# Optimization experiments

Hardware: AMD Instinct MI355X
Metric: run time of the kernel (lower is better)

The kernel has to match this reference:

```python
import jax, jax.numpy as jnp
import numpy as np

EPS = 1e-6
NEG_SLOPE = 0.01  # torch LeakyReLU default

def ln(x, g, b):
    m = jnp.mean(x, axis=-1, keepdims=True)
    v = jnp.mean((x - m) ** 2, axis=-1, keepdims=True)
    return (x - m) / jnp.sqrt(v + EPS) * g + b

def leaky(x):
    return jnp.where(x >= 0, x, NEG_SLOPE * x)

def setup_inputs() -> dict:
    B, L, F, H, NH, LBL = 8, 1024, 1024, 256, 8, 4766
    key = jax.random.key(0)
    ks = jax.random.split(key, 16)
    def lin(k, i, o, s=0.03):
        kw, kb = jax.random.split(k)
        return jax.random.normal(kw, (i, o), jnp.float32) * s, jnp.zeros((o,), jnp.float32)
    w_in, b_in = lin(ks[0], F, H)
    w_h, b_h = lin(ks[1], H, H)
    a_w1, a_b1 = lin(ks[2], H, 64)
    a_w2, a_b2 = lin(ks[3], 64, NH)
    o_w1, o_b1 = lin(ks[4], NH * H, NH * H)
    o_w2, o_b2 = lin(ks[5], NH * H, LBL)
    CM = (jax.random.uniform(ks[6], (LBL, LBL)) < 0.002).astype(jnp.float32)
    CM = jnp.maximum(CM, jnp.eye(LBL, dtype=jnp.float32))
    return {
        'h_V': jax.random.normal(ks[7], (B, L, F), jnp.float32),
        'mask': jnp.ones((B, L), jnp.int32),
        'ln0_g': jnp.ones((F,), jnp.float32), 'ln0_b': jnp.zeros((F,), jnp.float32),
        'w_in': w_in, 'b_in': b_in,
        'ln1_g': jnp.ones((H,), jnp.float32), 'ln1_b': jnp.zeros((H,), jnp.float32),
        'w_h': w_h, 'b_h': b_h,
        'ln2_g': jnp.ones((H,), jnp.float32), 'ln2_b': jnp.zeros((H,), jnp.float32),
        'a_w1': a_w1, 'a_b1': a_b1,
        'a_lng': jnp.ones((64,), jnp.float32), 'a_lnb': jnp.zeros((64,), jnp.float32),
        'a_w2': a_w2, 'a_b2': a_b2,
        'o_w1': o_w1, 'o_b1': o_b1,
        'o_lng': jnp.ones((NH * H,), jnp.float32), 'o_lnb': jnp.zeros((NH * H,), jnp.float32),
        'o_w2': o_w2, 'o_b2': o_b2,
        'CM': CM,
    }

def reference(h_V, mask, ln0_g, ln0_b, w_in, b_in, ln1_g, ln1_b, w_h, b_h,
              ln2_g, ln2_b, a_w1, a_b1, a_lng, a_lnb, a_w2, a_b2,
              o_w1, o_b1, o_lng, o_lnb, o_w2, o_b2, CM):
    B = h_V.shape[0]
    # input + hidden blocks (eval mode: dropout is identity)
    x = ln(h_V, ln0_g, ln0_b)
    x = leaky(x @ w_in + b_in)
    x = ln(x, ln1_g, ln1_b)
    x = leaky(x @ w_h + b_h)
    x = ln(x, ln2_g, ln2_b)                      # [B,L,H]
    # multi-head attention pooling over sequence
    a = leaky(x @ a_w1 + a_b1)
    a = ln(a, a_lng, a_lnb)
    a = a @ a_w2 + a_b2                          # [B,L,NH]
    a = jnp.where(mask[:, :, None] == 0, jnp.float32(-1e9), a)
    a = jax.nn.softmax(a, axis=1)
    h = jnp.einsum('blh,bld->bhd', a, x).reshape(B, -1)  # [B,NH*H]
    # output block
    h = leaky(h @ o_w1 + o_b1)
    h = ln(h, o_lng, o_lnb)
    p = jax.nn.sigmoid(h @ o_w2 + o_b2)          # [B,LBL]
    # GO-hierarchy max-product propagation (eval path)
    out = jnp.max(p[:, None, :] * CM[None, :, :], axis=-1)  # [B,LBL]
    return out.astype(jnp.float32)
```

## Files before the change

kernel.cpp:

```cpp
#include <hip/hip_runtime.h>
#include <hip/hip_bf16.h>
#include <cstdint>

#define B_   8
#define L_   1024
#define F_   1024
#define H_   256
#define NH_  8
#define LBL_ 4766
#define M_   (B_*L_)
#define OD_  (NH_*H_)
#define NCM  (LBL_*LBL_)
#define MP_EPB 16384
#define MP_NB  ((NCM + MP_EPB - 1) / MP_EPB)

typedef unsigned short u16;
typedef unsigned int   u32;
typedef __attribute__((ext_vector_type(8))) short short8;
typedef __attribute__((ext_vector_type(4))) float float4v;

#define BF16_ONES_PAIR 0x3f803f80u

__device__ __forceinline__ float bf2f(u32 u) { return __uint_as_float(u << 16); }
__device__ __forceinline__ u16 f2bf(float f) {
    u32 u = __float_as_uint(f);
    u32 r = 0x7fffu + ((u >> 16) & 1u);
    return (u16)((u + r) >> 16);
}

struct f8 { float v[8]; };

__device__ __forceinline__ float ldS(const void* p, size_t i, bool bf) {
    return bf ? bf2f(((const u16*)p)[i]) : ((const float*)p)[i];
}
__device__ __forceinline__ float4 ld4(const void* p, size_t i, bool bf) {
    if (bf) {
        uint2 u = *(const uint2*)((const u16*)p + i);
        return make_float4(bf2f(u.x & 0xffff), bf2f(u.x >> 16),
                           bf2f(u.y & 0xffff), bf2f(u.y >> 16));
    }
    return *(const float4*)((const float*)p + i);
}
__device__ __forceinline__ f8 ld8(const void* p, size_t i, bool bf) {
    f8 r;
    if (bf) {
        uint4 u = *(const uint4*)((const u16*)p + i);
        r.v[0]=bf2f(u.x&0xffff); r.v[1]=bf2f(u.x>>16);
        r.v[2]=bf2f(u.y&0xffff); r.v[3]=bf2f(u.y>>16);
        r.v[4]=bf2f(u.z&0xffff); r.v[5]=bf2f(u.z>>16);
        r.v[6]=bf2f(u.w&0xffff); r.v[7]=bf2f(u.w>>16);
    } else {
        const float* q = (const float*)p + i;
        float4 a = *(const float4*)q, b = *(const float4*)(q+4);
        r.v[0]=a.x; r.v[1]=a.y; r.v[2]=a.z; r.v[3]=a.w;
        r.v[4]=b.x; r.v[5]=b.y; r.v[6]=b.z; r.v[7]=b.w;
    }
    return r;
}

__device__ __forceinline__ float wave_sum(float v) {
    #pragma unroll
    for (int m = 1; m < 64; m <<= 1) v += __shfl_xor(v, m, 64);
    return v;
}
__device__ __forceinline__ float wave_max(float v) {
    #pragma unroll
    for (int m = 1; m < 64; m <<= 1) v = fmaxf(v, __shfl_xor(v, m, 64));
    return v;
}
__device__ __forceinline__ float blk_sum(float v, float* sh) {
    v = wave_sum(v);
    int w = threadIdx.x >> 6, nw = blockDim.x >> 6;
    if ((threadIdx.x & 63) == 0) sh[w] = v;
    __syncthreads();
    float s = sh[0];
    for (int i = 1; i < nw; ++i) s += sh[i];
    __syncthreads();
    return s;
}
__device__ __forceinline__ float blk_max(float v, float* sh) {
    v = wave_max(v);
    int w = threadIdx.x >> 6, nw = blockDim.x >> 6;
    if ((threadIdx.x & 63) == 0) sh[w] = v;
    __syncthreads();
    float s = sh[0];
    for (int i = 1; i < nw; ++i) s = fmaxf(s, sh[i]);
    __syncthreads();
    return s;
}

__global__ __launch_bounds__(256) void prep_k(const void* __restrict__ hv,
        const void* __restrict__ g0, const void* __restrict__ b0, u16* __restrict__ x0,
        const void* __restrict__ w_in, u16* __restrict__ wt1,
        const void* __restrict__ w_h,  u16* __restrict__ wt2,
        const void* __restrict__ aw1,  u16* __restrict__ wt3,
        float* __restrict__ zA, float* __restrict__ zB,
        const u32* __restrict__ probe) {
    __shared__ u16 tile[64][65];
    __shared__ float sh[4];
    bool bf = (probe[0] == BF16_ONES_PAIR);
    int blk = blockIdx.x, t = threadIdx.x;
    if (blk < M_) {
        float4 v = ld4(hv, (size_t)blk * F_ + t * 4, bf);
        float s = v.x + v.y + v.z + v.w;
        float q = v.x*v.x + v.y*v.y + v.z*v.z + v.w*v.w;
        s = blk_sum(s, sh);
        q = blk_sum(q, sh);
        float mean = s * (1.f / F_);
        float rstd = rsqrtf(q * (1.f / F_) - mean * mean + 1e-6f);
        float4 gg = ld4(g0, t * 4, bf);
        float4 bb = ld4(b0, t * 4, bf);
        u32 o0 = f2bf((v.x - mean) * rstd * gg.x + bb.x)
               | ((u32)f2bf((v.y - mean) * rstd * gg.y + bb.y) << 16);
        u32 o1 = f2bf((v.z - mean) * rstd * gg.z + bb.z)
               | ((u32)f2bf((v.w - mean) * rstd * gg.w + bb.w) << 16);
        *(uint2*)(x0 + (size_t)blk * F_ + t * 4) = make_uint2(o0, o1);
        return;
    }
    blk -= M_;
    const void* W = nullptr; u16* WT = nullptr; int K = 0, N = 0, kt = 0, nt = 0;
    if (blk < 64)      { W = w_in; WT = wt1; K = F_; N = H_; kt = blk & 15; nt = blk >> 4; }
    else if (blk < 80) { int j = blk - 64; W = w_h; WT = wt2; K = H_; N = H_; kt = j & 3; nt = j >> 2; }
    else if (blk < 84) { int j = blk - 80; W = aw1; WT = wt3; K = H_; N = 64; kt = j; nt = 0; }
    else {
        int j = blk - 84;
        if (j < 16) {
            float4* p = (float4*)zA;
            for (int i = j * 256 + t; i < 8192; i += 4096) p[i] = make_float4(0,0,0,0);
        } else {
            j -= 16;
            float4* p = (float4*)zB;
            for (int i = j * 256 + t; i < 13628; i += 4096) p[i] = make_float4(0,0,0,0);
        }
        return;
    }
    int kt0 = kt * 64, nt0 = nt * 64;
    int r = t >> 2, cq = (t & 3) * 16;
    #pragma unroll
    for (int j = 0; j < 4; ++j) {
        float4 v = ld4(W, (size_t)(kt0 + r) * N + nt0 + cq + j * 4, bf);
        tile[r][cq + j*4 + 0] = f2bf(v.x);
        tile[r][cq + j*4 + 1] = f2bf(v.y);
        tile[r][cq + j*4 + 2] = f2bf(v.z);
        tile[r][cq + j*4 + 3] = f2bf(v.w);
    }
    __syncthreads();
    #pragma unroll
    for (int j = 0; j < 4; ++j) {
        int k = cq + j * 4;
        u32 a0 = tile[k+0][r], a1 = tile[k+1][r], a2 = tile[k+2][r], a3 = tile[k+3][r];
        uint2 o; o.x = a0 | (a1 << 16); o.y = a2 | (a3 << 16);
        *(uint2*)(WT + (size_t)(nt0 + r) * K + kt0 + k) = o;
    }
}

__global__ __launch_bounds__(256) void gemm_mfma(const u16* __restrict__ Ap, int amode,
        const float2* __restrict__ statin, const void* __restrict__ g,
        const void* __restrict__ bta, const u16* __restrict__ WT,
        const void* __restrict__ bias, u16* __restrict__ C,
        float* __restrict__ statout, int M, int N, int K,
        const u32* __restrict__ probe) {
    __shared__ short8 As[64][5];
    __shared__ short8 Bs[64][5];
    bool pbf = (probe[0] == BF16_ONES_PAIR);
    int t = threadIdx.x;
    int m0 = blockIdx.x * 64, n0 = blockIdx.y * 64;
    int r = t >> 2, kq = t & 3;
    int l = t & 63, w = t >> 6;
    int q = l >> 4, ml = l & 15;
    float4v acc[4];
    #pragma unroll
    for (int nt = 0; nt < 4; ++nt)
        #pragma unroll
        for (int i = 0; i < 4; ++i) acc[nt][i] = 0.f;
    float stm = 0.f, str = 1.f;
    if (amode == 1) {
        float2 st = statin[m0 + r];
        float mm = st.x * (1.f / K);
        stm = mm;
        str = rsqrtf(st.y * (1.f / K) - mm * mm + 1e-6f);
    }
    for (int k0 = 0; k0 < K; k0 += 32) {
        int kk = k0 + kq * 8;
        short8 pa;
        if (amode == 1) {
            f8 a  = ld8(Ap, (size_t)(m0 + r) * K + kk, true);
            f8 gg = ld8(g, kk, pbf);
            f8 bb = ld8(bta, kk, pbf);
            #pragma unroll
            for (int j = 0; j < 8; ++j)
                pa[j] = (short)f2bf((a.v[j] - stm) * str * gg.v[j] + bb.v[j]);
        } else {
            pa = *(const short8*)(Ap + (size_t)(m0 + r) * K + kk);
        }
        short8 pb = *(const short8*)(WT + (size_t)(n0 + r) * K + kk);
        __syncthreads();
        As[r][kq] = pa;
        Bs[r][kq] = pb;
        __syncthreads();
        short8 af = As[w * 16 + ml][q];
        #pragma unroll
        for (int nt = 0; nt < 4; ++nt)
            acc[nt] = __builtin_amdgcn_mfma_f32_16x16x32_bf16(af, Bs[nt*16 + ml][q],
                                                              acc[nt], 0, 0, 0);
    }
    float ov[4][4];
    #pragma unroll
    for (int nt = 0; nt < 4; ++nt) {
        int nn = n0 + nt * 16 + ml;
        float bv = ldS(bias, nn, pbf);
        #pragma unroll
        for (int reg = 0; reg < 4; ++reg) {
            float v = acc[nt][reg] + bv;
            v = v >= 0.f ? v : 0.01f * v;
            ov[nt][reg] = v;
            C[(size_t)(m0 + w * 16 + q * 4 + reg) * N + nn] = f2bf(v);
        }
    }
    if (statout) {
        #pragma unroll
        for (int reg = 0; reg < 4; ++reg) {
            float sv = ov[0][reg] + ov[1][reg] + ov[2][reg] + ov[3][reg];
            float qv = ov[0][reg]*ov[0][reg] + ov[1][reg]*ov[1][reg]
                     + ov[2][reg]*ov[2][reg] + ov[3][reg]*ov[3][reg];
            #pragma unroll
            for (int mk = 1; mk < 16; mk <<= 1) {
                sv += __shfl_xor(sv, mk, 64);
                qv += __shfl_xor(qv, mk, 64);
            }
            if (ml == 0) {
                int row = m0 + w * 16 + q * 4 + reg;
                atomicAdd(&statout[2 * row],     sv);
                atomicAdd(&statout[2 * row + 1], qv);
            }
        }
    }
}

__global__ __launch_bounds__(256) void gemm3_attn_k(const u16* __restrict__ Ap,
        const float2* __restrict__ statin, const void* __restrict__ g,
        const void* __restrict__ bta, const u16* __restrict__ WT,
        const void* __restrict__ bias,
        const void* __restrict__ alng, const void* __restrict__ alnb,
        const void* __restrict__ aw2, const void* __restrict__ ab2,
        const int* __restrict__ mask, float* __restrict__ lg,
        const u32* __restrict__ probe) {
    __shared__ short8 As[64][5];
    __shared__ short8 Bs[64][5];
    __shared__ float at[64][65];
    __shared__ float w2s[512];
    __shared__ float b2s[8];
    __shared__ float gs[64], bs[64];
    bool pbf = (probe[0] == BF16_ONES_PAIR);
    const int K = 256;
    int t = threadIdx.x;
    int m0 = blockIdx.x * 64;
    int r = t >> 2, kq = t & 3;
    int l = t & 63, w = t >> 6;
    int q = l >> 4, ml = l & 15;
    float4v acc[4];
    #pragma unroll
    for (int nt = 0; nt < 4; ++nt)
        #pragma unroll
        for (int i = 0; i < 4; ++i) acc[nt][i] = 0.f;
    float2 st = statin[m0 + r];
    float stm = st.x * (1.f / K);
    float str = rsqrtf(st.y * (1.f / K) - stm * stm + 1e-6f);
    for (int k0 = 0; k0 < K; k0 += 32) {
        int kk = k0 + kq * 8;
        f8 a  = ld8(Ap, (size_t)(m0 + r) * K + kk, true);
        f8 gg = ld8(g, kk, pbf);
        f8 bb = ld8(bta, kk, pbf);
        short8 pa;
        #pragma unroll
        for (int j = 0; j < 8; ++j)
            pa[j] = (short)f2bf((a.v[j] - stm) * str * gg.v[j] + bb.v[j]);
        short8 pb = *(const short8*)(WT + (size_t)r * K + kk);
        __syncthreads();
        As[r][kq] = pa;
        Bs[r][kq] = pb;
        __syncthreads();
        short8 af = As[w * 16 + ml][q];
        #pragma unroll
        for (int nt = 0; nt < 4; ++nt)
            acc[nt] = __builtin_amdgcn_mfma_f32_16x16x32_bf16(af, Bs[nt*16 + ml][q],
                                                              acc[nt], 0, 0, 0);
    }
    for (int i = t; i < 512; i += 256) w2s[i] = ldS(aw2, i, pbf);
    if (t < 8) b2s[t] = ldS(ab2, t, pbf);
    if (t < 64) { gs[t] = ldS(alng, t, pbf); bs[t] = ldS(alnb, t, pbf); }
    #pragma unroll
    for (int nt = 0; nt < 4; ++nt) {
        int nn = nt * 16 + ml;
        float bv = ldS(bias, nn, pbf);
        #pragma unroll
        for (int reg = 0; reg < 4; ++reg) {
            float v = acc[nt][reg] + bv;
            v = v >= 0.f ? v : 0.01f * v;
            at[w * 16 + q * 4 + reg][nn] = v;
        }
    }
    __syncthreads();
    int row = t >> 2, s4 = t & 3;
    float av[16];
    float sum = 0.f, sq = 0.f;
    #pragma unroll
    for (int j = 0; j < 16; ++j) {
        float v = at[row][s4 * 16 + j];
        av[j] = v; sum += v; sq += v * v;
    }
    sum += __shfl_xor(sum, 1, 64); sum += __shfl_xor(sum, 2, 64);
    sq  += __shfl_xor(sq, 1, 64);  sq  += __shfl_xor(sq, 2, 64);
    float mr = sum * (1.f / 64);
    float rr = rsqrtf(sq * (1.f / 64) - mr * mr + 1e-6f);
    float val[16];
    #pragma unroll
    for (int j = 0; j < 16; ++j)
        val[j] = (av[j] - mr) * rr * gs[s4 * 16 + j] + bs[s4 * 16 + j];
    float hv[8];
    #pragma unroll
    for (int h = 0; h < 8; ++h) {
        float p = 0.f;
        #pragma unroll
        for (int j = 0; j < 16; ++j) p += val[j] * w2s[(s4 * 16 + j) * 8 + h];
        p += __shfl_xor(p, 1, 64);
        p += __shfl_xor(p, 2, 64);
        hv[h] = p + b2s[h];
    }
    if (s4 == 0) {
        int gr = m0 + row;
        bool mz = (mask[gr] == 0);
        int bb_ = gr >> 10, ll = gr & 1023;
        #pragma unroll
        for (int h = 0; h < 8; ++h) {
            float v = mz ? -1e9f : hv[h];
            lg[((size_t)bb_ * NH_ + h) * L_ + ll] = v;
        }
    }
}

__global__ __launch_bounds__(1024) void attnpool_k(const float* __restrict__ lg,
        const float2* __restrict__ st2, const u16* __restrict__ x2,
        const void* __restrict__ g, const void* __restrict__ b,
        float* __restrict__ hp, const u32* __restrict__ probe) {
    __shared__ float aw_s[1024];
    __shared__ float part[16][256];
    __shared__ float sh[16];
    bool pbf = (probe[0] == BF16_ONES_PAIR);
    int bh = blockIdx.x, t = threadIdx.x;
    int bb = bh >> 3;
    float v = lg[(size_t)bh * L_ + t];
    float mx = blk_max(v, sh);
    float e = expf(v - mx);
    float s = blk_sum(e, sh);
    float inv = 1.f / s;
    float2 st = st2[(bb << 10) + t];
    float m = st.x * (1.f / 256);
    float r = rsqrtf(st.y * (1.f / 256) - m * m + 1e-6f);
    float aw = e * inv * r;
    aw_s[t] = aw;
    float c1 = blk_sum(aw * m, sh);
    int chunk = t >> 6, d0 = (t & 63) * 4;
    const u16* xb = x2 + ((size_t)(bb << 10) + chunk * 64) * 256;
    const float* awc = aw_s + chunk * 64;
    float a0 = 0.f, a1 = 0.f, a2 = 0.f, a3 = 0.f;
    #pragma unroll 8
    for (int i = 0; i < 64; ++i) {
        uint2 u = *(const uint2*)(xb + (size_t)i * 256 + d0);
        float wv = awc[i];
        a0 += wv * bf2f(u.x & 0xffff);
        a1 += wv * bf2f(u.x >> 16);
        a2 += wv * bf2f(u.y & 0xffff);
        a3 += wv * bf2f(u.y >> 16);
    }
    *(float4*)&part[chunk][d0] = make_float4(a0, a1, a2, a3);
    __syncthreads();
    if (t < 256) {
        float S = 0.f;
        #pragma unroll
        for (int c = 0; c < 16; ++c) S += part[c][t];
        hp[(size_t)bh * 256 + t] = (S - c1) * ldS(g, t, pbf) + ldS(b, t, pbf);
    }
}

__global__ __launch_bounds__(256) void gemv2_k(const float* __restrict__ hv,
        const void* __restrict__ W, float* __restrict__ acc, int K, int N,
        const u32* __restrict__ probe) {
    __shared__ float hs[8 * 64];
    bool bf = (probe[0] == BF16_ONES_PAIR);
    int t = threadIdx.x;
    int kb = blockIdx.y * 64;
    for (int i = t; i < 512; i += 256) {
        int r = i >> 6, k = i & 63;
        hs[i] = hv[(size_t)r * K + kb + k];
    }
    __syncthreads();
    int c0 = (blockIdx.x * 256 + t) * 2;
    if (c0 >= N) return;
    float a[8][2] = {};
    #pragma unroll 4
    for (int k = 0; k < 64; ++k) {
        float w0, w1;
        if (bf) {
            u32 u = *(const u32*)((const u16*)W + (size_t)(kb + k) * N + c0);
            w0 = bf2f(u & 0xffff); w1 = bf2f(u >> 16);
        } else {
            float2 fw = *(const float2*)((const float*)W + (size_t)(kb + k) * N + c0);
            w0 = fw.x; w1 = fw.y;
        }
        #pragma unroll
        for (int r = 0; r < 8; ++r) {
            float h = hs[(r << 6) + k];
            a[r][0] += h * w0; a[r][1] += h * w1;
        }
    }
    bool ok1 = (c0 + 1 < N);
    #pragma unroll
    for (int r = 0; r < 8; ++r) {
        atomicAdd(&acc[(size_t)r * N + c0], a[r][0]);
        if (ok1) atomicAdd(&acc[(size_t)r * N + c0 + 1], a[r][1]);
    }
}

__global__ __launch_bounds__(256) void out_ln_k(float* __restrict__ h,
        const void* __restrict__ bias, const void* __restrict__ g,
        const void* __restrict__ b, const u32* __restrict__ probe) {
    __shared__ float sh[4];
    bool bf = (probe[0] == BF16_ONES_PAIR);
    int row = blockIdx.x, t = threadIdx.x;
    float v[8];
    float s = 0.f, q = 0.f;
    #pragma unroll
    for (int i = 0; i < 8; ++i) {
        int c = t + i * 256;
        float x = h[(size_t)row * OD_ + c] + ldS(bias, c, bf);
        x = x >= 0.f ? x : 0.01f * x;
        v[i] = x; s += x; q += x * x;
    }
    s = blk_sum(s, sh) * (1.f / OD_);
    q = blk_sum(q, sh) * (1.f / OD_);
    float rstd = rsqrtf(q - s * s + 1e-6f);
    #pragma unroll
    for (int i = 0; i < 8; ++i) {
        int c = t + i * 256;
        h[(size_t)row * OD_ + c] = (v[i] - s) * rstd * ldS(g, c, bf) + ldS(b, c, bf);
    }
}

__global__ __launch_bounds__(256) void sigmoid_t_k(const float* __restrict__ acc,
        const void* __restrict__ bias, float* __restrict__ pt,
        float* __restrict__ out, const u32* __restrict__ probe) {
    bool bf = (probe[0] == BF16_ONES_PAIR);
    int c = blockIdx.x * 256 + threadIdx.x;
    if (c >= LBL_) return;
    float bv = ldS(bias, c, bf);
    float o[8];
    #pragma unroll
    for (int r = 0; r < 8; ++r) {
        float v = acc[(size_t)r * LBL_ + c] + bv;
        o[r] = 1.f / (1.f + expf(-v));
        out[(size_t)r * LBL_ + c] = 0.f;
    }
    float4* dst = (float4*)(pt + (size_t)c * 8);
    dst[0] = make_float4(o[0], o[1], o[2], o[3]);
    dst[1] = make_float4(o[4], o[5], o[6], o[7]);
}

__device__ __forceinline__ void mp_hit(u32 idx, float cmv,
        const float* __restrict__ pt, int* smax, u32 rowBase) {
    u32 i = idx / LBL_;
    u32 j = idx - i * LBL_;
    const float4* pj = (const float4*)(pt + (size_t)j * 8);
    float4 pa = pj[0], pb = pj[1];
    int base = (int)(i - rowBase) * 8;
    atomicMax(&smax[base + 0], __float_as_int(pa.x * cmv));
    atomicMax(&smax[base + 1], __float_as_int(pa.y * cmv));
    atomicMax(&smax[base + 2], __float_as_int(pa.z * cmv));
    atomicMax(&smax[base + 3], __float_as_int(pa.w * cmv));
    atomicMax(&smax[base + 4], __float_as_int(pb.x * cmv));
    atomicMax(&smax[base + 5], __float_as_int(pb.y * cmv));
    atomicMax(&smax[base + 6], __float_as_int(pb.z * cmv));
    atomicMax(&smax[base + 7], __float_as_int(pb.w * cmv));
}

__global__ __launch_bounds__(256) void maxprod3_k(const float* __restrict__ pt,
        const void* __restrict__ CM, float* __restrict__ out,
        const u32* __restrict__ probe) {
    __shared__ int smax[6 * 8];
    bool bf = (probe[0] == BF16_ONES_PAIR);
    int t = threadIdx.x;
    size_t blockStart = (size_t)blockIdx.x * MP_EPB;
    u32 rowBase = (u32)(blockStart / LBL_);
    for (int i = t; i < 48; i += 256) smax[i] = 0;
    __syncthreads();
    if (bf) {
        const u16* cm = (const u16*)CM;
        uint4 ch[8];
        size_t i0[8];
        #pragma unroll
        for (int u = 0; u < 8; ++u) {
            size_t idx0 = blockStart + ((size_t)u * 256 + t) * 8;
            i0[u] = idx0;
            ch[u] = (idx0 + 8 <= NCM) ? *(const uint4*)(cm + idx0)
                                      : make_uint4(0, 0, 0, 0);
        }
        #pragma unroll
        for (int u = 0; u < 8; ++u) {
            size_t idx0 = i0[u];
            if (idx0 + 8 <= NCM) {
                uint4 c4 = ch[u];
                if ((c4.x | c4.y | c4.z | c4.w) == 0) continue;
                u32 hw[4] = {c4.x, c4.y, c4.z, c4.w};
                #pragma unroll
                for (int d = 0; d < 4; ++d) {
                    u32 lo = hw[d] & 0xffff, hi = hw[d] >> 16;
                    if (lo) mp_hit((u32)idx0 + d*2,     bf2f(lo), pt, smax, rowBase);
                    if (hi) mp_hit((u32)idx0 + d*2 + 1, bf2f(hi), pt, smax, rowBase);
                }
            } else if (idx0 < NCM) {
                for (u32 e = 0; e < (u32)(NCM - idx0); ++e) {
                    u16 h = cm[idx0 + e];
                    if (h) mp_hit((u32)idx0 + e, bf2f(h), pt, smax, rowBase);
                }
            }
        }
    } else {
        const float* cm = (const float*)CM;
        #pragma unroll
        for (int u = 0; u < 16; ++u) {
            size_t idx0 = blockStart + ((size_t)u * 256 + t) * 4;
            if (idx0 >= NCM) continue;
            float v[4];
            if (idx0 + 4 <= NCM) {
                float4 f = *(const float4*)(cm + idx0);
                v[0] = f.x; v[1] = f.y; v[2] = f.z; v[3] = f.w;
            } else {
                v[0] = v[1] = v[2] = v[3] = 0.f;
                for (u32 e = 0; e < (u32)(NCM - idx0); ++e) v[e] = cm[idx0 + e];
            }
            if (v[0] == 0.f && v[1] == 0.f && v[2] == 0.f && v[3] == 0.f) continue;
            #pragma unroll
            for (int e = 0; e < 4; ++e)
                if (v[e] != 0.f) mp_hit((u32)idx0 + e, v[e], pt, smax, rowBase);
        }
    }
    __syncthreads();
    size_t lastIdx = blockStart + MP_EPB - 1;
    if (lastIdx >= NCM) lastIdx = NCM - 1;
    int nrows = (int)((u32)(lastIdx / LBL_) - rowBase) + 1;
    for (int s = t; s < nrows * 8; s += 256) {
        int v = smax[s];
        if (v != 0) {
            int rr = s >> 3, b = s & 7;
            atomicMax((int*)(out + (size_t)b * LBL_ + rowBase + rr), v);
        }
    }
}

extern "C" void kernel_launch(void* const* d_in, const int* in_sizes, int n_in,
                              void* d_out, int out_size, void* d_ws, size_t ws_size,
                              hipStream_t stream) {
    const void* hv   = d_in[0];
    const int* mask  = (const int*)d_in[1];
    const void* ln0g = d_in[2];
    const void* ln0b = d_in[3];
    const void* w_in = d_in[4];
    const void* b_in = d_in[5];
    const void* ln1g = d_in[6];
    const void* ln1b = d_in[7];
    const void* w_h  = d_in[8];
    const void* b_h  = d_in[9];
    const void* ln2g = d_in[10];
    const void* ln2b = d_in[11];
    const void* aw1  = d_in[12];
    const void* ab1  = d_in[13];
    const void* alng = d_in[14];
    const void* alnb = d_in[15];
    const void* aw2  = d_in[16];
    const void* ab2  = d_in[17];
    const void* ow1  = d_in[18];
    const void* ob1  = d_in[19];
    const void* olng = d_in[20];
    const void* olnb = d_in[21];
    const void* ow2  = d_in[22];
    const void* ob2  = d_in[23];
    const void* CM   = d_in[24];
    const u32* probe = (const u32*)ln0g;
    float* out = (float*)d_out;

    float* f = (float*)d_ws;
    float2* st1 = (float2*)f;
    float2* st2 = st1 + 8192;
    float* lg = f + 32768;
    float* c1 = lg + 65536;
    float* Sp = c1 + 64;
    float* hp = Sp + 131072;
    float* ha = hp + 16384;
    float* l2 = ha + 16384;
    float* pt = l2 + 38128;
    u16* x0  = (u16*)(pt + 38128);
    u16* x1  = x0 + 8388608;
    u16* x2  = x1 + 2097152;
    u16* abr = x2 + 2097152;
    u16* wt1 = abr + 524288;
    u16* wt2 = wt1 + 262144;
    u16* wt3 = wt2 + 65536;

    prep_k<<<M_ + 84 + 32, 256, 0, stream>>>(hv, ln0g, ln0b, x0,
                                             w_in, wt1, w_h, wt2, aw1, wt3,
                                             f, ha, probe);
    gemm_mfma<<<dim3(M_/64, 4), 256, 0, stream>>>(x0, 2, nullptr, nullptr, nullptr,
                                                  wt1, b_in, x1, (float*)st1,
                                                  M_, H_, F_, probe);
    gemm_mfma<<<dim3(M_/64, 4), 256, 0, stream>>>(x1, 1, st1, ln1g, ln1b,
                                                  wt2, b_h, x2, (float*)st2,
                                                  M_, H_, H_, probe);
    gemm3_attn_k<<<M_/64, 256, 0, stream>>>(x2, st2, ln2g, ln2b, wt3, ab1,
                                            alng, alnb, aw2, ab2, mask, lg, probe);
    attnpool_k<<<B_*NH_, 1024, 0, stream>>>(lg, st2, x2, ln2g, ln2b, hp, probe);
    gemv2_k<<<dim3(OD_/512, 32), 256, 0, stream>>>(hp, ow1, ha, OD_, OD_, probe);
    out_ln_k<<<B_, 256, 0, stream>>>(ha, ob1, olng, olnb, probe);
    gemv2_k<<<dim3((LBL_+511)/512, 32), 256, 0, stream>>>(ha, ow2, l2, OD_, LBL_, probe);
    sigmoid_t_k<<<(LBL_+255)/256, 256, 0, stream>>>(l2, ob2, pt, out, probe);
    maxprod3_k<<<MP_NB, 256, 0, stream>>>(pt, CM, out, probe);
}
```

Baseline: 353.7 us.

## Double-buffer GEMM LDS tiles, wave-per-row input LayerNorm, 4-wide output GEMV

```diff
diff --git a/kernel.cpp b/kernel.cpp
--- a/kernel.cpp
+++ b/kernel.cpp
@@ -97,27 +97,40 @@
         float* __restrict__ zA, float* __restrict__ zB,
         const u32* __restrict__ probe) {
     __shared__ u16 tile[64][65];
-    __shared__ float sh[4];
     bool bf = (probe[0] == BF16_ONES_PAIR);
     int blk = blockIdx.x, t = threadIdx.x;
-    if (blk < M_) {
-        float4 v = ld4(hv, (size_t)blk * F_ + t * 4, bf);
-        float s = v.x + v.y + v.z + v.w;
-        float q = v.x*v.x + v.y*v.y + v.z*v.z + v.w*v.w;
-        s = blk_sum(s, sh);
-        q = blk_sum(q, sh);
+    if (blk < M_/4) {
+        int row = (blk << 2) + (t >> 6);
+        int l = t & 63;
+        size_t base = (size_t)row * F_;
+        float4 vv[4];
+        float s = 0.f, q = 0.f;
+        #pragma unroll
+        for (int j = 0; j < 4; ++j) {
+            float4 v = ld4(hv, base + l * 4 + j * 256, bf);
+            vv[j] = v;
+            s += v.x + v.y + v.z + v.w;
+            q += v.x*v.x + v.y*v.y + v.z*v.z + v.w*v.w;
+        }
+        s = wave_sum(s);
+        q = wave_sum(q);
         float mean = s * (1.f / F_);
         float rstd = rsqrtf(q * (1.f / F_) - mean * mean + 1e-6f);
-        float4 gg = ld4(g0, t * 4, bf);
-        float4 bb = ld4(b0, t * 4, bf);
-        u32 o0 = f2bf((v.x - mean) * rstd * gg.x + bb.x)
-               | ((u32)f2bf((v.y - mean) * rstd * gg.y + bb.y) << 16);
-        u32 o1 = f2bf((v.z - mean) * rstd * gg.z + bb.z)
-               | ((u32)f2bf((v.w - mean) * rstd * gg.w + bb.w) << 16);
-        *(uint2*)(x0 + (size_t)blk * F_ + t * 4) = make_uint2(o0, o1);
+        #pragma unroll
+        for (int j = 0; j < 4; ++j) {
+            int off = l * 4 + j * 256;
+            float4 gg = ld4(g0, off, bf);
+            float4 bb = ld4(b0, off, bf);
+            float4 v = vv[j];
+            u32 o0 = f2bf((v.x - mean) * rstd * gg.x + bb.x)
+                   | ((u32)f2bf((v.y - mean) * rstd * gg.y + bb.y) << 16);
+            u32 o1 = f2bf((v.z - mean) * rstd * gg.z + bb.z)
+                   | ((u32)f2bf((v.w - mean) * rstd * gg.w + bb.w) << 16);
+            *(uint2*)(x0 + base + off) = make_uint2(o0, o1);
+        }
         return;
     }
-    blk -= M_;
+    blk -= M_/4;
     const void* W = nullptr; u16* WT = nullptr; int K = 0, N = 0, kt = 0, nt = 0;
     if (blk < 64)      { W = w_in; WT = wt1; K = F_; N = H_; kt = blk & 15; nt = blk >> 4; }
     else if (blk < 80) { int j = blk - 64; W = w_h; WT = wt2; K = H_; N = H_; kt = j & 3; nt = j >> 2; }
@@ -160,8 +173,8 @@
         const void* __restrict__ bias, u16* __restrict__ C,
         float* __restrict__ statout, int M, int N, int K,
         const u32* __restrict__ probe) {
-    __shared__ short8 As[64][5];
-    __shared__ short8 Bs[64][5];
+    __shared__ short8 As[2][64][5];
+    __shared__ short8 Bs[2][64][5];
     bool pbf = (probe[0] == BF16_ONES_PAIR);
     int t = threadIdx.x;
     int m0 = blockIdx.x * 64, n0 = blockIdx.y * 64;
@@ -180,29 +193,48 @@
         stm = mm;
         str = rsqrtf(st.y * (1.f / K) - mm * mm + 1e-6f);
     }
-    for (int k0 = 0; k0 < K; k0 += 32) {
-        int kk = k0 + kq * 8;
-        short8 pa;
+    const size_t arow = (size_t)(m0 + r) * K;
+    const size_t brow = (size_t)(n0 + r) * K;
+    auto loadA = [&](int kk) -> short8 {
         if (amode == 1) {
-            f8 a  = ld8(Ap, (size_t)(m0 + r) * K + kk, true);
+            f8 a  = ld8(Ap, arow + kk, true);
             f8 gg = ld8(g, kk, pbf);
             f8 bb = ld8(bta, kk, pbf);
+            short8 pa;
             #pragma unroll
             for (int j = 0; j < 8; ++j)
                 pa[j] = (short)f2bf((a.v[j] - stm) * str * gg.v[j] + bb.v[j]);
-        } else {
-            pa = *(const short8*)(Ap + (size_t)(m0 + r) * K + kk);
-        }
-        short8 pb = *(const short8*)(WT + (size_t)(n0 + r) * K + kk);
-        __syncthreads();
-        As[r][kq] = pa;
-        Bs[r][kq] = pb;
-        __syncthreads();
-        short8 af = As[w * 16 + ml][q];
+            return pa;
+        }
+        return *(const short8*)(Ap + arow + kk);
+    };
+    {
+        short8 pa = loadA(kq * 8);
+        short8 pb = *(const short8*)(WT + brow + kq * 8);
+        As[0][r][kq] = pa;
+        Bs[0][r][kq] = pb;
+    }
+    __syncthreads();
+    int nIt = K >> 5, cur = 0;
+    for (int it = 0; it < nIt; ++it) {
+        bool more = (it + 1 < nIt);
+        short8 na, nb;
+        if (more) {
+            int kk = (it + 1) * 32 + kq * 8;
+            na = loadA(kk);
+            nb = *(const short8*)(WT + brow + kk);
+        }
+        short8 af = As[cur][w * 16 + ml][q];
         #pragma unroll
         for (int nt = 0; nt < 4; ++nt)
-            acc[nt] = __builtin_amdgcn_mfma_f32_16x16x32_bf16(af, Bs[nt*16 + ml][q],
+            acc[nt] = __builtin_amdgcn_mfma_f32_16x16x32_bf16(af, Bs[cur][nt*16 + ml][q],
                                                               acc[nt], 0, 0, 0);
+        if (more) {
+            As[cur ^ 1][r][kq] = na;
+            Bs[cur ^ 1][r][kq] = nb;
+            __syncthreads();
+            cur ^= 1;
+        }
     }
     float ov[4][4];
     #pragma unroll
@@ -245,8 +277,8 @@
         const void* __restrict__ aw2, const void* __restrict__ ab2,
         const int* __restrict__ mask, float* __restrict__ lg,
         const u32* __restrict__ probe) {
-    __shared__ short8 As[64][5];
-    __shared__ short8 Bs[64][5];
+    __shared__ short8 As[2][64][5];
+    __shared__ short8 Bs[2][64][5];
     __shared__ float at[64][65];
     __shared__ float w2s[512];
     __shared__ float b2s[8];
@@ -266,25 +298,46 @@
     float2 st = statin[m0 + r];
     float stm = st.x * (1.f / K);
     float str = rsqrtf(st.y * (1.f / K) - stm * stm + 1e-6f);
-    for (int k0 = 0; k0 < K; k0 += 32) {
-        int kk = k0 + kq * 8;
-        f8 a  = ld8(Ap, (size_t)(m0 + r) * K + kk, true);
+    const size_t arow = (size_t)(m0 + r) * K;
+    const size_t brow = (size_t)r * K;
+    auto loadA = [&](int kk) -> short8 {
+        f8 a  = ld8(Ap, arow + kk, true);
         f8 gg = ld8(g, kk, pbf);
         f8 bb = ld8(bta, kk, pbf);
         short8 pa;
         #pragma unroll
         for (int j = 0; j < 8; ++j)
             pa[j] = (short)f2bf((a.v[j] - stm) * str * gg.v[j] + bb.v[j]);
-        short8 pb = *(const short8*)(WT + (size_t)r * K + kk);
-        __syncthreads();
-        As[r][kq] = pa;
-        Bs[r][kq] = pb;
-        __syncthreads();
-        short8 af = As[w * 16 + ml][q];
+        return pa;
+    };
+    {
+        short8 pa = loadA(kq * 8);
+        short8 pb = *(const short8*)(WT + brow + kq * 8);
+        As[0][r][kq] = pa;
+        Bs[0][r][kq] = pb;
+    }
+    __syncthreads();
+    int cur = 0;
+    #pragma unroll
+    for (int it = 0; it < 8; ++it) {
+        bool more = (it < 7);
+        short8 na, nb;
+        if (more) {
+            int kk = (it + 1) * 32 + kq * 8;
+            na = loadA(kk);
+            nb = *(const short8*)(WT + brow + kk);
+        }
+        short8 af = As[cur][w * 16 + ml][q];
         #pragma unroll
         for (int nt = 0; nt < 4; ++nt)
-            acc[nt] = __builtin_amdgcn_mfma_f32_16x16x32_bf16(af, Bs[nt*16 + ml][q],
+            acc[nt] = __builtin_amdgcn_mfma_f32_16x16x32_bf16(af, Bs[cur][nt*16 + ml][q],
                                                               acc[nt], 0, 0, 0);
+        if (more) {
+            As[cur ^ 1][r][kq] = na;
+            Bs[cur ^ 1][r][kq] = nb;
+            __syncthreads();
+            cur ^= 1;
+        }
     }
     for (int i = t; i < 512; i += 256) w2s[i] = ldS(aw2, i, pbf);
     if (t < 8) b2s[t] = ldS(ab2, t, pbf);
@@ -422,6 +475,60 @@
     }
 }
 
+__global__ __launch_bounds__(256) void gemv4_k(const float* __restrict__ hv,
+        const void* __restrict__ W, float* __restrict__ acc, int K, int N,
+        const u32* __restrict__ probe) {
+    __shared__ float hs[8 * 64];
+    bool bf = (probe[0] == BF16_ONES_PAIR);
+    int t = threadIdx.x;
+    int kb = blockIdx.y * 64;
+    for (int i = t; i < 512; i += 256) {
+        int r = i >> 6, k = i & 63;
+        hs[i] = hv[(size_t)r * K + kb + k];
+    }
+    __syncthreads();
+    int c0 = (blockIdx.x * 256 + t) * 4;
+    if (c0 >= N) return;
+    float a[8][4] = {};
+    if (c0 + 4 <= N) {
+        #pragma unroll 2
+        for (int k = 0; k < 64; ++k) {
+            float w0, w1, w2, w3;
+            if (bf) {
+                uint2 u = *(const uint2*)((const u16*)W + (size_t)(kb + k) * N + c0);
+                w0 = bf2f(u.x & 0xffff); w1 = bf2f(u.x >> 16);
+                w2 = bf2f(u.y & 0xffff); w3 = bf2f(u.y >> 16);
+            } else {
+                float4 fw = *(const float4*)((const float*)W + (size_t)(kb + k) * N + c0);
+                w0 = fw.x; w1 = fw.y; w2 = fw.z; w3 = fw.w;
+            }
+            #pragma unroll
+            for (int r = 0; r < 8; ++r) {
+                float h = hs[(r << 6) + k];
+                a[r][0] += h * w0; a[r][1] += h * w1;
+                a[r][2] += h * w2; a[r][3] += h * w3;
+            }
+        }
+    } else {
+        int ncol = N - c0;
+        for (int k = 0; k < 64; ++k) {
+            #pragma unroll
+            for (int e = 0; e < 4; ++e) {
+                if (e < ncol) {
+                    float wv = ldS(W, (size_t)(kb + k) * N + c0 + e, bf);
+                    #pragma unroll
+                    for (int r = 0; r < 8; ++r) a[r][e] += hs[(r << 6) + k] * wv;
+                }
+            }
+        }
+    }
+    #pragma unroll
+    for (int r = 0; r < 8; ++r)
+        #pragma unroll
+        for (int e = 0; e < 4; ++e)
+            if (c0 + e < N) atomicAdd(&acc[(size_t)r * N + c0 + e], a[r][e]);
+}
+
 __global__ __launch_bounds__(256) void out_ln_k(float* __restrict__ h,
         const void* __restrict__ bias, const void* __restrict__ g,
         const void* __restrict__ b, const u32* __restrict__ probe) {
@@ -606,9 +713,9 @@
     u16* wt2 = wt1 + 262144;
     u16* wt3 = wt2 + 65536;
 
-    prep_k<<<M_ + 84 + 32, 256, 0, stream>>>(hv, ln0g, ln0b, x0,
-                                             w_in, wt1, w_h, wt2, aw1, wt3,
-                                             f, ha, probe);
+    prep_k<<<M_/4 + 84 + 32, 256, 0, stream>>>(hv, ln0g, ln0b, x0,
+                                               w_in, wt1, w_h, wt2, aw1, wt3,
+                                               f, ha, probe);
     gemm_mfma<<<dim3(M_/64, 4), 256, 0, stream>>>(x0, 2, nullptr, nullptr, nullptr,
                                                   wt1, b_in, x1, (float*)st1,
                                                   M_, H_, F_, probe);
@@ -620,7 +727,7 @@
     attnpool_k<<<B_*NH_, 1024, 0, stream>>>(lg, st2, x2, ln2g, ln2b, hp, probe);
     gemv2_k<<<dim3(OD_/512, 32), 256, 0, stream>>>(hp, ow1, ha, OD_, OD_, probe);
     out_ln_k<<<B_, 256, 0, stream>>>(ha, ob1, olng, olnb, probe);
-    gemv2_k<<<dim3((LBL_+511)/512, 32), 256, 0, stream>>>(ha, ow2, l2, OD_, LBL_, probe);
+    gemv4_k<<<dim3((LBL_+1023)/1024, 32), 256, 0, stream>>>(ha, ow2, l2, OD_, LBL_, probe);
     sigmoid_t_k<<<(LBL_+255)/256, 256, 0, stream>>>(l2, ob2, pt, out, probe);
     maxprod3_k<<<MP_NB, 256, 0, stream>>>(pt, CM, out, probe);
 }
```

Result: slower. 384.1 us (+8.6%).
